# Kernel optimization log

Hardware: AMD Instinct MI355X
Metric: run time of the kernel (lower is better)

Reference implementation:

```python
import jax, jax.numpy as jnp
import numpy as np

TAU = 0.5      # init kwarg tau
LAMBD = 0.5    # init kwarg lambd
N, D, C = 4096, 1024, 512


def setup_inputs() -> dict:
    key = jax.random.key(0)
    k1, k2, k3 = jax.random.split(key, 3)
    return {
        "layer_embeds": jax.random.normal(k1, (N, D), dtype=jnp.float32),
        "y_true": jax.random.randint(k2, (N,), 0, C),
        "y_pred": jax.random.normal(k3, (N, C), dtype=jnp.float32),
    }


def _clce(x, y_true, y_pred):
    n = x.shape[0]
    # pairwise cosine similarity via one matmul (torch eps = 1e-8)
    norms = jnp.clip(jnp.linalg.norm(x, axis=1, keepdims=True), 1e-8)
    xn = x / norms
    sim = (xn @ xn.T + 1.0) * 0.5 * TAU          # [N, N]

    same = y_true[:, None] == y_true[None, :]    # diagonal is always True
    eye = jnp.eye(n, dtype=bool)
    pos_mask = same & ~eye                        # candidate positives (j != i)
    neg_mask = ~same                              # negatives (excludes diagonal)

    # slot 0: similarity to the FIRST positive j (in j order), else stays 0
    first_pos = jnp.argmax(pos_mask, axis=1)
    has_pos = pos_mask.any(axis=1)
    slot0 = jnp.where(has_pos,
                      jnp.take_along_axis(sim, first_pos[:, None], axis=1)[:, 0],
                      0.0)

    # negatives packed left-to-right into columns 1..; unfilled slots stay 0
    cum = jnp.cumsum(neg_mask, axis=1)            # 1-based slot per negative
    cols = jnp.where(neg_mask, cum, 2 * n - 1)    # non-negatives -> sink col
    rows = jnp.arange(n)[:, None]
    loss_temp = jnp.zeros((n, 2 * n), dtype=sim.dtype)
    loss_temp = loss_temp.at[rows, cols].add(jnp.where(neg_mask, sim, 0.0))
    loss_temp = loss_temp.at[:, 0].set(slot0)
    loss_temp = loss_temp[:, : 2 * n - 1]         # drop sink column -> [N, 2N-1]

    cl = -jax.nn.log_softmax(loss_temp, axis=1)[:, 0]
    cl = cl.sum() / n

    logp = jax.nn.log_softmax(y_pred, axis=1)
    ce = -jnp.take_along_axis(logp, y_true[:, None], axis=1).mean()

    return LAMBD * cl + (1.0 - LAMBD) * ce


def reference(layer_embeds, y_true, y_pred):
    return _clce(layer_embeds, y_true, y_pred)
```

## Files before the change

### kernel.cpp

```cpp
#include <hip/hip_runtime.h>
#include <hip/hip_bf16.h>
#include <hip/hip_fp8.h>

#define NR 4096
#define DIM 1024
#define NCLS 512

typedef __attribute__((ext_vector_type(4))) float f32x4;
typedef __attribute__((ext_vector_type(2))) long i64x2;

__global__ __launch_bounds__(256) void k_prep(const float* __restrict__ x,
                                              const int* __restrict__ y,
                                              const float* __restrict__ yp,
                                              unsigned char* __restrict__ xnp,
                                              int* __restrict__ cnt,
                                              int* __restrict__ fpos,
                                              float* __restrict__ slot0,
                                              float* __restrict__ ce,
                                              float* __restrict__ out) {
  const int b = blockIdx.x;
  const int tid = threadIdx.x;
  if (b < 1024) {
    int row = b * 4 + (tid >> 6);
    int lane = tid & 63;
    const float4* xr = reinterpret_cast<const float4*>(x + (size_t)row * DIM);
    float4 v[4];
    float s = 0.f;
#pragma unroll
    for (int it = 0; it < 4; ++it) {
      v[it] = xr[it * 64 + lane];
      s += v[it].x * v[it].x + v[it].y * v[it].y + v[it].z * v[it].z + v[it].w * v[it].w;
    }
#pragma unroll
    for (int d = 1; d < 64; d <<= 1) s += __shfl_xor(s, d);
    float inv = 64.0f / fmaxf(sqrtf(s), 1e-8f);
    unsigned char* xo = xnp + (size_t)row * DIM;
#pragma unroll
    for (int it = 0; it < 4; ++it) {
      int k0q = it * 64 + lane;
      int kt = k0q >> 4;
      int r6 = (k0q & 15) * 4;
      int p = ((r6 & 31) >> 3) * 16 + (r6 >> 5) * 8 + (r6 & 7);
      __hip_fp8_e4m3 b0(v[it].x * inv), b1(v[it].y * inv),
                     b2(v[it].z * inv), b3(v[it].w * inv);
      unsigned int pk = (unsigned int)b0.__x | ((unsigned int)b1.__x << 8) |
                        ((unsigned int)b2.__x << 16) | ((unsigned int)b3.__x << 24);
      *(unsigned int*)(xo + kt * 64 + p) = pk;
    }
  } else if (b < 2048) {
    int row = (b - 1024) * 4 + (tid >> 6);
    int lane = tid & 63;
    const float4* p = reinterpret_cast<const float4*>(yp + (size_t)row * NCLS);
    float4 v0 = p[lane], v1 = p[lane + 64];
    float m = fmaxf(fmaxf(fmaxf(v0.x, v0.y), fmaxf(v0.z, v0.w)),
                    fmaxf(fmaxf(v1.x, v1.y), fmaxf(v1.z, v1.w)));
#pragma unroll
    for (int d = 1; d < 64; d <<= 1) m = fmaxf(m, __shfl_xor(m, d));
    float s = __expf(v0.x - m) + __expf(v0.y - m) + __expf(v0.z - m) + __expf(v0.w - m) +
              __expf(v1.x - m) + __expf(v1.y - m) + __expf(v1.z - m) + __expf(v1.w - m);
#pragma unroll
    for (int d = 1; d < 64; d <<= 1) s += __shfl_xor(s, d);
    if (lane == 0) {
      float py = yp[(size_t)row * NCLS + y[row]];
      ce[row] = logf(s) + m - py;
    }
  } else {
    __shared__ int ys[NR];
    __shared__ int scnt[NCLS], sm1[NCLS], sm2[NCLS];
    for (int j = tid; j < NR; j += 256) ys[j] = y[j];
    for (int c = tid; c < NCLS; c += 256) { scnt[c] = 0; sm1[c] = NR; sm2[c] = NR; }
    __syncthreads();
    for (int i = tid; i < NR; i += 256) {
      int c = ys[i];
      atomicAdd(&scnt[c], 1);
      atomicMin(&sm1[c], i);
    }
    __syncthreads();
    for (int i = tid; i < NR; i += 256) {
      int c = ys[i];
      if (sm1[c] != i) atomicMin(&sm2[c], i);
    }
    __syncthreads();
    for (int i = tid; i < NR; i += 256) {
      int c = ys[i];
      int m1 = sm1[c];
      int j = (m1 == i) ? ((sm2[c] >= NR) ? -1 : sm2[c]) : m1;
      fpos[i] = j;
      slot0[i] = 0.f;
    }
    for (int c = tid; c < NCLS; c += 256) cnt[c] = scnt[c];
    if (tid == 0) out[0] = 0.f;
  }
}


#define STAGE(SSLOT, GROWBASE, KT)                                               \
  {                                                                              \
    const char* _src = (const char*)xnp +                                        \
        (size_t)((GROWBASE) + srow) * 1024 + (size_t)(KT) * 64 + scol;           \
    __builtin_amdgcn_global_load_lds(                                            \
        (const __attribute__((address_space(1))) void*)_src,                     \
        (__attribute__((address_space(3))) void*)(lds + (SSLOT) + (w << 10)),    \
        16, 0, 0);                                                               \
  }

#define PHASE(BUFB, MF0, LOADB, SSLOT, SBASE, SKT, VM)                           \
  {                                                                              \
    _Pragma("unroll") for (int mm = 0; mm < 2; ++mm)                             \
      afr[mm] = *(const i64x2*)(lds + (BUFB) + ABaseW +                          \
                                ((MF0) + mm) * 1024 + kread);                    \
    if (LOADB) {                                                                 \
      _Pragma("unroll") for (int nf = 0; nf < 4; ++nf)                           \
        bfr[nf] = *(const i64x2*)(lds + (BUFB) + BBaseW + nf * 1024 + kread);    \
    }                                                                            \
    STAGE(SSLOT, SBASE, SKT)                                                     \
    if (VM) asm volatile("s_waitcnt vmcnt(2)" ::: "memory");                     \
    __builtin_amdgcn_s_barrier();                                                \
    asm volatile("s_waitcnt lgkmcnt(0)" ::: "memory");                           \
    __builtin_amdgcn_sched_barrier(0);                                           \
    __builtin_amdgcn_s_setprio(1);                                               \
    _Pragma("unroll") for (int kk = 0; kk < 2; ++kk)                             \
      _Pragma("unroll") for (int mm = 0; mm < 2; ++mm)                           \
        _Pragma("unroll") for (int nf = 0; nf < 4; ++nf)                         \
          acc[(MF0) + mm][nf] = __builtin_amdgcn_mfma_f32_16x16x32_fp8_fp8(      \
              afr[mm][kk], bfr[nf][kk], acc[(MF0) + mm][nf], 0, 0, 0);           \
    __builtin_amdgcn_s_setprio(0);                                               \
    __builtin_amdgcn_sched_barrier(0);                                           \
    __builtin_amdgcn_s_barrier();                                                \
  }

__global__ __launch_bounds__(512, 2) void k_gemm(const unsigned char* __restrict__ xnp,
                                                 const int* __restrict__ y,
                                                 const int* __restrict__ fpos,
                                                 float* __restrict__ part,
                                                 float* __restrict__ slot0) {
  __shared__ char lds[65536];
  const int tid = threadIdx.x;
  const int w = tid >> 6, lane = tid & 63;
  const int wr = w >> 2, wcn = w & 3;
  const int r0 = lane & 15, klo = lane >> 4;

  const int bid = blockIdx.x;
  const int swzb = (bid & 7) * 32 + (bid >> 3);
  const int rb = swzb >> 4, cb = swzb & 15;
  const int rowbase = rb * 256, colbase = cb * 256;

  const int kread = (klo * 16) ^ ((r0 & 3) << 4);
  const int ABaseW = wr * 8192 + r0 * 64;
  const int BBaseW = 16384 + (wcn >> 1) * 8192 + (wcn & 1) * 4096 + r0 * 64;

  int srow, scol;
  {
    int D = tid * 16;
    int L = D ^ (((D >> 6) & 3) << 4);
    srow = L >> 6;
    scol = L & 63;
  }

  f32x4 acc[8][4] = {};

  STAGE(0, rowbase, 0)
  STAGE(8192, rowbase + 128, 0)
  STAGE(16384, colbase, 0)
  STAGE(24576, colbase + 128, 0)
  STAGE(32768 + 16384, colbase, 1)
  STAGE(32768 + 24576, colbase + 128, 1)
  asm volatile("s_waitcnt vmcnt(2)" ::: "memory");
  __builtin_amdgcn_s_barrier();

  for (int i = 0; i < 8; ++i) {
    const int t1 = 2 * i + 1;
    const int tn0 = (2 * i + 2 < 16) ? 2 * i + 2 : 15;
    const int tn1 = (2 * i + 3 < 16) ? 2 * i + 3 : 15;
    i64x2 afr[2], bfr[4];
    PHASE(0, 0, 1, 32768, rowbase, t1, 0)
    PHASE(0, 2, 0, 32768 + 8192, rowbase + 128, t1, 0)
    PHASE(0, 4, 0, 16384, colbase, tn0, 0)
    PHASE(0, 6, 0, 24576, colbase + 128, tn0, 1)
    PHASE(32768, 0, 1, 0, rowbase, tn0, 0)
    PHASE(32768, 2, 0, 8192, rowbase + 128, tn0, 0)
    PHASE(32768, 4, 0, 32768 + 16384, colbase, tn1, 0)
    PHASE(32768, 6, 0, 32768 + 24576, colbase + 128, tn1, 1)
  }

  asm volatile("s_waitcnt vmcnt(0)" ::: "memory");
  __syncthreads();

  int* yrow_s = (int*)lds;
  int* ycol_s = (int*)(lds + 1024);
  int* frow_s = (int*)(lds + 2048);
  float* rsum = (float*)(lds + 4096);
  if (tid < 256) {
    yrow_s[tid] = y[rowbase + tid];
    frow_s[tid] = fpos[rowbase + tid];
  } else {
    ycol_s[tid - 256] = y[colbase + tid - 256];
  }
  __syncthreads();

  const int g = klo;
#pragma unroll
  for (int mf = 0; mf < 8; ++mf) {
    float rs[4] = {0.f, 0.f, 0.f, 0.f};
    int rloc[4], yr[4], fr[4];
#pragma unroll
    for (int reg = 0; reg < 4; ++reg) {
      rloc[reg] = wr * 128 + mf * 16 + g * 4 + reg;
      yr[reg] = yrow_s[rloc[reg]];
      fr[reg] = frow_s[rloc[reg]];
    }
#pragma unroll
    for (int nf = 0; nf < 4; ++nf) {
      int cl = wcn * 64 + nf * 16 + r0;
      int yc = ycol_s[cl];
      int gc = colbase + cl;
#pragma unroll
      for (int reg = 0; reg < 4; ++reg) {
        float sv = acc[mf][nf][reg] * (1.0f / 16384.f) + 0.25f;
        float e = (yr[reg] == yc) ? 0.f : __expf(sv);
        rs[reg] += e;
        if (fr[reg] == gc) slot0[rowbase + rloc[reg]] = sv;
      }
    }
#pragma unroll
    for (int d = 1; d < 16; d <<= 1)
#pragma unroll
      for (int reg = 0; reg < 4; ++reg) rs[reg] += __shfl_xor(rs[reg], d);
    if (r0 == 0) {
#pragma unroll
      for (int reg = 0; reg < 4; ++reg)
        rsum[rloc[reg] * 4 + wcn] = rs[reg];
    }
  }
  __syncthreads();
  if (tid < 256)
    part[(size_t)cb * NR + rowbase + tid] =
        rsum[tid * 4] + rsum[tid * 4 + 1] + rsum[tid * 4 + 2] + rsum[tid * 4 + 3];
}

__global__ __launch_bounds__(256) void k_final(const float* __restrict__ part,
                                               const float* __restrict__ slot0,
                                               const int* __restrict__ cnt,
                                               const int* __restrict__ y,
                                               const float* __restrict__ ce,
                                               float* __restrict__ out) {
  __shared__ float red[256];
  const int tid = threadIdx.x;
  const int r = blockIdx.x * 256 + tid;
  float S = 0.f;
#pragma unroll
  for (int b = 0; b < 16; ++b) S += part[(size_t)b * NR + r];
  float s0 = slot0[r];
  float zeros = 4094.0f + (float)cnt[y[r]];
  float cl = logf(__expf(s0) + S + zeros) - s0;
  red[tid] = 0.5f * (cl + ce[r]);
  __syncthreads();
  for (int s = 128; s > 0; s >>= 1) {
    if (tid < s) red[tid] += red[tid + s];
    __syncthreads();
  }
  if (tid == 0) atomicAdd(out, red[0] / (float)NR);
}

extern "C" void kernel_launch(void* const* d_in, const int* in_sizes, int n_in,
                              void* d_out, int out_size, void* d_ws, size_t ws_size,
                              hipStream_t stream) {
  const float* x = (const float*)d_in[0];
  const int* y = (const int*)d_in[1];
  const float* yp = (const float*)d_in[2];
  float* out = (float*)d_out;

  char* w = (char*)d_ws;
  unsigned char* xnp = (unsigned char*)w;
  int* cnt = (int*)(w + 4194304);
  int* fpos = (int*)(w + 4196352);
  float* slot0 = (float*)(w + 4212736);
  float* part = (float*)(w + 4229120);
  float* ce = (float*)(w + 4491264);

  k_prep<<<2049, 256, 0, stream>>>(x, y, yp, xnp, cnt, fpos, slot0, ce, out);
  k_gemm<<<256, 512, 0, stream>>>(xnp, y, fpos, part, slot0);
  k_final<<<16, 256, 0, stream>>>(part, slot0, cnt, y, ce, out);
}
```

Measured before the change: 49.10 us.

## Quantize normalized embeddings to FP4 and use scaled FP4 MFMA for Gram matrix

The prep kernel now quantizes normalized embeddings to 4-bit e2m1 codes with a hand-written rounding function, packing two codes per byte in a layout matching the MFMA operand order. The GEMM switches from the FP8 16x16x32 MFMA to the scaled 16x16x128 f8f6f4 MFMA in FP4 mode with unit scales, halving the K loop and the bytes staged per row. This targets the GEMM's compute and memory-traffic cost, but FP4 quantization adds large rounding error to the similarities and may push the loss past tolerance.

```diff
diff --git a/kernel.cpp b/kernel.cpp
--- a/kernel.cpp
+++ b/kernel.cpp
@@ -1,13 +1,27 @@
 #include <hip/hip_runtime.h>
 #include <hip/hip_bf16.h>
-#include <hip/hip_fp8.h>
 
 #define NR 4096
 #define DIM 1024
 #define NCLS 512
 
 typedef __attribute__((ext_vector_type(4))) float f32x4;
-typedef __attribute__((ext_vector_type(2))) long i64x2;
+typedef __attribute__((ext_vector_type(8))) int v8i;
+
+static __device__ __forceinline__ unsigned int q4(float v) {
+  unsigned int s = (v < 0.f) ? 8u : 0u;
+  float a = fabsf(v);
+  unsigned int c;
+  if (a < 0.25f) c = 0;
+  else if (a < 0.75f) c = 1;
+  else if (a < 1.25f) c = 2;
+  else if (a < 1.75f) c = 3;
+  else if (a < 2.5f) c = 4;
+  else if (a < 3.5f) c = 5;
+  else if (a < 5.0f) c = 6;
+  else c = 7;
+  return s | c;
+}
 
 __global__ __launch_bounds__(256) void k_prep(const float* __restrict__ x,
                                               const int* __restrict__ y,
@@ -33,19 +47,17 @@
     }
 #pragma unroll
     for (int d = 1; d < 64; d <<= 1) s += __shfl_xor(s, d);
-    float inv = 64.0f / fmaxf(sqrtf(s), 1e-8f);
-    unsigned char* xo = xnp + (size_t)row * DIM;
+    float inv = 32.0f / fmaxf(sqrtf(s), 1e-8f);
+    unsigned char* xo = xnp + (size_t)row * 512;
 #pragma unroll
     for (int it = 0; it < 4; ++it) {
-      int k0q = it * 64 + lane;
-      int kt = k0q >> 4;
-      int r6 = (k0q & 15) * 4;
-      int p = ((r6 & 31) >> 3) * 16 + (r6 >> 5) * 8 + (r6 & 7);
-      __hip_fp8_e4m3 b0(v[it].x * inv), b1(v[it].y * inv),
-                     b2(v[it].z * inv), b3(v[it].w * inv);
-      unsigned int pk = (unsigned int)b0.__x | ((unsigned int)b1.__x << 8) |
-                        ((unsigned int)b2.__x << 16) | ((unsigned int)b3.__x << 24);
-      *(unsigned int*)(xo + kt * 64 + p) = pk;
+      int k0 = (it * 64 + lane) * 4;
+      int pos = (k0 >> 7) * 64 + ((k0 >> 5) & 3) * 16 + ((k0 & 31) >> 1);
+      unsigned int n0 = q4(v[it].x * inv), n1 = q4(v[it].y * inv),
+                   n2 = q4(v[it].z * inv), n3 = q4(v[it].w * inv);
+      unsigned short pk =
+          (unsigned short)(n0 | (n1 << 4) | (n2 << 8) | (n3 << 12));
+      *(unsigned short*)(xo + pos) = pk;
     }
   } else if (b < 2048) {
     int row = (b - 1024) * 4 + (tid >> 6);
@@ -97,7 +109,7 @@
 #define STAGE(SSLOT, GROWBASE, KT)                                               \
   {                                                                              \
     const char* _src = (const char*)xnp +                                        \
-        (size_t)((GROWBASE) + srow) * 1024 + (size_t)(KT) * 64 + scol;           \
+        (size_t)((GROWBASE) + srow) * 512 + (size_t)(KT) * 64 + scol;            \
     __builtin_amdgcn_global_load_lds(                                            \
         (const __attribute__((address_space(1))) void*)_src,                     \
         (__attribute__((address_space(3))) void*)(lds + (SSLOT) + (w << 10)),    \
@@ -106,12 +118,18 @@
 
 #define PHASE(BUFB, MF0, LOADB, SSLOT, SBASE, SKT, VM)                           \
   {                                                                              \
-    _Pragma("unroll") for (int mm = 0; mm < 2; ++mm)                             \
-      afr[mm] = *(const i64x2*)(lds + (BUFB) + ABaseW +                          \
-                                ((MF0) + mm) * 1024 + kread);                    \
+    _Pragma("unroll") for (int mm = 0; mm < 2; ++mm) {                           \
+      int4 t4 = *(const int4*)(lds + (BUFB) + ABaseW +                           \
+                               ((MF0) + mm) * 1024 + kread);                     \
+      v8i tv = {t4.x, t4.y, t4.z, t4.w, 0, 0, 0, 0};                             \
+      afr[mm] = tv;                                                              \
+    }                                                                            \
     if (LOADB) {                                                                 \
-      _Pragma("unroll") for (int nf = 0; nf < 4; ++nf)                           \
-        bfr[nf] = *(const i64x2*)(lds + (BUFB) + BBaseW + nf * 1024 + kread);    \
+      _Pragma("unroll") for (int nf = 0; nf < 4; ++nf) {                         \
+        int4 t4 = *(const int4*)(lds + (BUFB) + BBaseW + nf * 1024 + kread);     \
+        v8i tv = {t4.x, t4.y, t4.z, t4.w, 0, 0, 0, 0};                           \
+        bfr[nf] = tv;                                                            \
+      }                                                                          \
     }                                                                            \
     STAGE(SSLOT, SBASE, SKT)                                                     \
     if (VM) asm volatile("s_waitcnt vmcnt(2)" ::: "memory");                     \
@@ -119,11 +137,11 @@
     asm volatile("s_waitcnt lgkmcnt(0)" ::: "memory");                           \
     __builtin_amdgcn_sched_barrier(0);                                           \
     __builtin_amdgcn_s_setprio(1);                                               \
-    _Pragma("unroll") for (int kk = 0; kk < 2; ++kk)                             \
-      _Pragma("unroll") for (int mm = 0; mm < 2; ++mm)                           \
-        _Pragma("unroll") for (int nf = 0; nf < 4; ++nf)                         \
-          acc[(MF0) + mm][nf] = __builtin_amdgcn_mfma_f32_16x16x32_fp8_fp8(      \
-              afr[mm][kk], bfr[nf][kk], acc[(MF0) + mm][nf], 0, 0, 0);           \
+    _Pragma("unroll") for (int mm = 0; mm < 2; ++mm)                             \
+      _Pragma("unroll") for (int nf = 0; nf < 4; ++nf)                           \
+        acc[(MF0) + mm][nf] = __builtin_amdgcn_mfma_scale_f32_16x16x128_f8f6f4(  \
+            afr[mm], bfr[nf], acc[(MF0) + mm][nf], 4, 4,                         \
+            0, 0x7F7F7F7F, 0, 0x7F7F7F7F);                                       \
     __builtin_amdgcn_s_setprio(0);                                               \
     __builtin_amdgcn_sched_barrier(0);                                           \
     __builtin_amdgcn_s_barrier();                                                \
@@ -168,11 +186,11 @@
   asm volatile("s_waitcnt vmcnt(2)" ::: "memory");
   __builtin_amdgcn_s_barrier();
 
-  for (int i = 0; i < 8; ++i) {
+  for (int i = 0; i < 4; ++i) {
     const int t1 = 2 * i + 1;
-    const int tn0 = (2 * i + 2 < 16) ? 2 * i + 2 : 15;
-    const int tn1 = (2 * i + 3 < 16) ? 2 * i + 3 : 15;
-    i64x2 afr[2], bfr[4];
+    const int tn0 = (2 * i + 2 < 8) ? 2 * i + 2 : 7;
+    const int tn1 = (2 * i + 3 < 8) ? 2 * i + 3 : 7;
+    v8i afr[2], bfr[4];
     PHASE(0, 0, 1, 32768, rowbase, t1, 0)
     PHASE(0, 2, 0, 32768 + 8192, rowbase + 128, t1, 0)
     PHASE(0, 4, 0, 16384, colbase, tn0, 0)
@@ -216,7 +234,7 @@
       int gc = colbase + cl;
 #pragma unroll
       for (int reg = 0; reg < 4; ++reg) {
-        float sv = acc[mf][nf][reg] * (1.0f / 16384.f) + 0.25f;
+        float sv = acc[mf][nf][reg] * (1.0f / 4096.f) + 0.25f;
         float e = (yr[reg] == yc) ? 0.f : __expf(sv);
         rs[reg] += e;
         if (fr[reg] == gc) slot0[rowbase + rloc[reg]] = sv;
@@ -272,11 +290,11 @@
 
   char* w = (char*)d_ws;
   unsigned char* xnp = (unsigned char*)w;
-  int* cnt = (int*)(w + 4194304);
-  int* fpos = (int*)(w + 4196352);
-  float* slot0 = (float*)(w + 4212736);
-  float* part = (float*)(w + 4229120);
-  float* ce = (float*)(w + 4491264);
+  int* cnt = (int*)(w + 2097152);
+  int* fpos = (int*)(w + 2099200);
+  float* slot0 = (float*)(w + 2115584);
+  float* part = (float*)(w + 2131968);
+  float* ce = (float*)(w + 2394112);
 
   k_prep<<<2049, 256, 0, stream>>>(x, y, yp, xnp, cnt, fpos, slot0, ce, out);
   k_gemm<<<256, 512, 0, stream>>>(xnp, y, fpos, part, slot0);
```

After: 87.44 us. +78.1%, slower.
